# Kernel optimization log

Measured on AMD Instinct MI355X. Metric: run time of the kernel, lower is better.

The kernel has to match this reference:

```python
import jax, jax.numpy as jnp
import numpy as np

NEG_INF = -9e15
ALPHA = 0.2  # LeakyReLU negative slope


def setup_inputs() -> dict:
    key = jax.random.key(0)
    k1, k2, k3, k4 = jax.random.split(key, 4)
    B, N, C_IN, C_OUT, H = 8, 2048, 256, 256, 4
    node_feats = jax.random.normal(k1, (B, N, C_IN), dtype=jnp.float32)
    adj_matrix = jax.random.randint(k2, (B, N, N), 0, 2, dtype=jnp.int32)
    # include self-connections as the docstring expects
    eye = jnp.eye(N, dtype=jnp.int32)[None]
    adj_matrix = jnp.maximum(adj_matrix, eye)
    W = jax.random.normal(k3, (C_OUT, C_IN), dtype=jnp.float32) * (1.414 / np.sqrt(C_IN))
    b = jnp.zeros((C_OUT,), dtype=jnp.float32)
    a = jax.random.normal(k4, (H, 2 * (C_OUT // H)), dtype=jnp.float32) * 0.1
    return {"node_feats": node_feats, "adj_matrix": adj_matrix, "W": W, "b": b, "a": a}


def reference(node_feats, adj_matrix, W, b, a):
    B, N, _ = node_feats.shape
    H, two_c = a.shape
    c = two_c // 2
    # projection: [B, N, H, c]
    f = (jnp.einsum('bni,oi->bno', node_feats, W) + b).reshape(B, N, H, c)
    # attention logit for edge (i, j): leakyrelu(a . [f_i, f_j])
    # decomposes as leakyrelu(s_src[i] + s_dst[j])
    a_src, a_dst = a[:, :c], a[:, c:]
    s_src = jnp.einsum('bnhc,hc->bnh', f, a_src)  # [B, N, H]
    s_dst = jnp.einsum('bnhc,hc->bnh', f, a_dst)  # [B, N, H]
    logits = jax.nn.leaky_relu(s_src[:, :, None, :] + s_dst[:, None, :, :], ALPHA)  # [B,N,N,H]
    logits = jnp.where(adj_matrix[..., None] == 1, logits, NEG_INF)
    probs = jax.nn.softmax(logits, axis=2)  # softmax over source nodes j
    out = jnp.einsum('bijh,bjhc->bihc', probs, f)
    return out.reshape(B, N, H * c)  # concat_heads=True
```

## Files before the change

kernel.cpp:

```cpp
#include <hip/hip_runtime.h>

#define LOG2E 1.4426950408889634f

typedef __attribute__((ext_vector_type(8))) short short8;
typedef __attribute__((ext_vector_type(4))) float f32x4;

__device__ __forceinline__ unsigned short f2bf(float f) {
  unsigned int u = __float_as_uint(f);
  u = (u + 0x7fffu + ((u >> 16) & 1u)) >> 16;
  return (unsigned short)u;
}

__global__ __launch_bounds__(256) void gat_k1(
    const float* __restrict__ X, const float* __restrict__ W,
    const float* __restrict__ bias, const float* __restrict__ a,
    unsigned short* __restrict__ ft, float* __restrict__ ssrc,
    float* __restrict__ sdst)
{
  __shared__ float Xs[8][128];
  __shared__ float Ws[8][128];
  const int tid = threadIdx.x;
  const int tx = tid & 15, ty = tid >> 4;
  const int m0 = blockIdx.x * 128;
  const int c0 = blockIdx.y * 128;

  float acc[8][8];
#pragma unroll
  for (int r = 0; r < 8; ++r)
#pragma unroll
    for (int j = 0; j < 8; ++j) acc[r][j] = 0.f;

  const int lrow = tid >> 1;
  const int kk0 = (tid & 1) * 4;
  const float* Xp = X + (size_t)(m0 + lrow) * 256 + kk0;
  const float* Wp = W + (size_t)(c0 + lrow) * 256 + kk0;

  for (int kc = 0; kc < 256; kc += 8) {
    float4 xv = *(const float4*)(Xp + kc);
    float4 wv = *(const float4*)(Wp + kc);
    __syncthreads();
    Xs[kk0 + 0][lrow] = xv.x; Xs[kk0 + 1][lrow] = xv.y;
    Xs[kk0 + 2][lrow] = xv.z; Xs[kk0 + 3][lrow] = xv.w;
    Ws[kk0 + 0][lrow] = wv.x; Ws[kk0 + 1][lrow] = wv.y;
    Ws[kk0 + 2][lrow] = wv.z; Ws[kk0 + 3][lrow] = wv.w;
    __syncthreads();
#pragma unroll
    for (int kk = 0; kk < 8; ++kk) {
      float av[8], wv8[8];
#pragma unroll
      for (int r = 0; r < 8; ++r) av[r] = Xs[kk][ty * 8 + r];
#pragma unroll
      for (int j = 0; j < 8; ++j) wv8[j] = Ws[kk][tx * 8 + j];
#pragma unroll
      for (int r = 0; r < 8; ++r)
#pragma unroll
        for (int j = 0; j < 8; ++j) acc[r][j] = fmaf(av[r], wv8[j], acc[r][j]);
    }
  }

  const int b = m0 >> 11;
  const int nloc0 = (m0 & 2047) + ty * 8;
  const int cg0 = c0 + tx * 8;
  const int h = cg0 >> 6;
  const int cb = cg0 & 63;

  float bv[8], av_s[8], av_d[8];
#pragma unroll
  for (int j = 0; j < 8; ++j) {
    bv[j]   = bias[cg0 + j];
    av_s[j] = a[h * 128 + cb + j];
    av_d[j] = a[h * 128 + 64 + cb + j];
  }
#pragma unroll
  for (int r = 0; r < 8; ++r)
#pragma unroll
    for (int j = 0; j < 8; ++j) acc[r][j] += bv[j];

  const int jt = nloc0 >> 4;
  const int ni = nloc0 & 15;
#pragma unroll
  for (int j = 0; j < 8; ++j) {
    unsigned int u[4];
#pragma unroll
    for (int q = 0; q < 4; ++q) {
      unsigned int lo = f2bf(acc[2 * q + 0][j]);
      unsigned int hi = f2bf(acc[2 * q + 1][j]);
      u[q] = lo | (hi << 16);
    }
    size_t off = ((((size_t)b * 128 + jt) * 4 + h) * 64 + (cb + j)) * 16 + ni;
    *(uint4*)(ft + off) = make_uint4(u[0], u[1], u[2], u[3]);
  }

  float sp[8], dp[8];
#pragma unroll
  for (int r = 0; r < 8; ++r) {
    float s = 0.f, d = 0.f;
#pragma unroll
    for (int j = 0; j < 8; ++j) {
      s = fmaf(acc[r][j], av_s[j], s);
      d = fmaf(acc[r][j], av_d[j], d);
    }
    sp[r] = s; dp[r] = d;
  }
#pragma unroll
  for (int off = 1; off < 8; off <<= 1) {
#pragma unroll
    for (int r = 0; r < 8; ++r) {
      sp[r] += __shfl_xor(sp[r], off);
      dp[r] += __shfl_xor(dp[r], off);
    }
  }
  if ((tx & 7) == 0) {
    float* sb = ssrc + ((size_t)b * 4 + h) * 2048 + nloc0;
    float* db = sdst + ((size_t)b * 4 + h) * 2048 + nloc0;
#pragma unroll
    for (int r = 0; r < 8; ++r) { sb[r] = sp[r] * LOG2E; db[r] = dp[r] * LOG2E; }
  }
}

__global__ __launch_bounds__(512, 8) void gat_k2(
    const int* __restrict__ adj, const unsigned short* __restrict__ ft,
    const float* __restrict__ ssrc, const float* __restrict__ sdst,
    float* __restrict__ out)
{
  __shared__ __align__(16) unsigned char lds[37120];
  float* sd = (float*)lds;
  unsigned* Aw = (unsigned*)(lds + 32768);

  const int tid = threadIdx.x;
  const int b = blockIdx.x & 7;
  const int itile = blockIdx.x >> 3;
  const int i0 = itile * 16;
  const int w = tid >> 6;
  const int h = w >> 1;
  const int p = w & 1;
  const int lane = tid & 63;
  const int i_l = lane & 15;
  const int kg = lane >> 4;
  const int shamt = kg * 8;

  {
    const float4* src = (const float4*)(sdst + (size_t)b * 4 * 2048);
    float4* dst = (float4*)sd;
#pragma unroll
    for (int q = 0; q < 4; ++q) dst[tid + q * 512] = src[tid + q * 512];
  }
  {
    const int* abase = adj + (size_t)b * 2048 * 2048 + (size_t)i0 * 2048;
    unsigned short* dst16 = (unsigned short*)Aw;
#pragma unroll
    for (int k = 0; k < 4; ++k) {
      const int idx = k * 512 + tid;
      const int r = idx >> 7;
      const int s16 = idx & 127;
      const int4* ap = (const int4*)(abase + (size_t)r * 2048 + s16 * 16);
      int4 v0 = ap[0], v1 = ap[1], v2 = ap[2], v3 = ap[3];
      int vv[16] = {v0.x, v0.y, v0.z, v0.w, v1.x, v1.y, v1.z, v1.w,
                    v2.x, v2.y, v2.z, v2.w, v3.x, v3.y, v3.z, v3.w};
      unsigned m = 0;
#pragma unroll
      for (int i = 0; i < 16; ++i) m |= (vv[i] ? 1u : 0u) << i;
      dst16[((s16 >> 1) * 17 + r) * 2 + (s16 & 1)] = (unsigned short)m;
    }
  }
  const float si = ssrc[((size_t)b * 4 + h) * 2048 + i0 + i_l];
  const float* sdh = sd + h * 2048 + p * 1024 + kg * 8;
  const unsigned short* ftb =
      ft + ((((size_t)b * 128 + p * 64 + (kg >> 1)) * 4 + h) * 64 + i_l) * 16 +
      (kg & 1) * 8;

  f32x4 acc0, acc1, acc2, acc3;
#pragma unroll
  for (int q = 0; q < 4; ++q) { acc0[q] = 0.f; acc1[q] = 0.f; acc2[q] = 0.f; acc3[q] = 0.f; }
  float lsum = 0.f;

  __syncthreads();

#define COMP(s)                                                   \
  {                                                               \
    const unsigned wrd = Aw[(p * 32 + (s)) * 17 + i_l];           \
    const unsigned byte_ = (wrd >> shamt) & 0xffu;                \
    const float* tp_ = sdh + (s) * 32;                            \
    float4 t0_ = *(const float4*)tp_;                             \
    float4 t1_ = *(const float4*)(tp_ + 4);                       \
    float tj_[8] = {t0_.x, t0_.y, t0_.z, t0_.w,                   \
                    t1_.x, t1_.y, t1_.z, t1_.w};                  \
    float e_[8];                                                  \
    _Pragma("unroll")                                             \
    for (int q = 0; q < 8; ++q) {                                 \
      float x_ = si + tj_[q];                                     \
      float y_ = fmaxf(x_, 0.2f * x_);                            \
      float ev_ = __builtin_amdgcn_exp2f(y_);                     \
      ev_ = (byte_ & (1u << q)) ? ev_ : 0.f;                      \
      e_[q] = ev_;                                                \
      lsum += ev_;                                                \
    }                                                             \
    union { unsigned u[4]; short8 v; } af_;                       \
    _Pragma("unroll")                                             \
    for (int q2 = 0; q2 < 4; ++q2) {                              \
      unsigned r_;                                                \
      asm("v_cvt_pk_bf16_f32 %0, %1, %2"                          \
          : "=v"(r_) : "v"(e_[2 * q2]), "v"(e_[2 * q2 + 1]));     \
      af_.u[q2] = r_;                                             \
    }                                                             \
    const unsigned short* fp_ = ftb + (size_t)(s) * 8192;         \
    union { uint4 q; short8 v; } b0_, b1_, b2_, b3_;              \
    b0_.q = *(const uint4*)(fp_);                                 \
    b1_.q = *(const uint4*)(fp_ + 256);                           \
    b2_.q = *(const uint4*)(fp_ + 512);                           \
    b3_.q = *(const uint4*)(fp_ + 768);                           \
    acc0 = __builtin_amdgcn_mfma_f32_16x16x32_bf16(af_.v, b0_.v, acc0, 0, 0, 0); \
    acc1 = __builtin_amdgcn_mfma_f32_16x16x32_bf16(af_.v, b1_.v, acc1, 0, 0, 0); \
    acc2 = __builtin_amdgcn_mfma_f32_16x16x32_bf16(af_.v, b2_.v, acc2, 0, 0, 0); \
    acc3 = __builtin_amdgcn_mfma_f32_16x16x32_bf16(af_.v, b3_.v, acc3, 0, 0, 0); \
  }

#pragma unroll 4
  for (int s = 0; s < 32; ++s) {
    COMP(s)
  }
#undef COMP

  float lsum2 = lsum + __shfl_xor(lsum, 16);
  lsum2 += __shfl_xor(lsum2, 32);
  float* ep = (float*)lds;
  float* el = (float*)(lds + 16384);
  __syncthreads();
  if (p == 1) {
#pragma unroll
    for (int r = 0; r < 4; ++r) {
      const int row = kg * 4 + r;
      ep[(h * 16 + row) * 64 + 0  + i_l] = acc0[r];
      ep[(h * 16 + row) * 64 + 16 + i_l] = acc1[r];
      ep[(h * 16 + row) * 64 + 32 + i_l] = acc2[r];
      ep[(h * 16 + row) * 64 + 48 + i_l] = acc3[r];
    }
    if (lane < 16) el[h * 16 + lane] = lsum2;
  }
  __syncthreads();
  if (p == 0) {
    const float L = lsum2 + el[h * 16 + i_l];
    const float rinv = 1.0f / L;
    float* ob = out + ((size_t)(b * 2048 + i0)) * 256 + h * 64;
#pragma unroll
    for (int r = 0; r < 4; ++r) {
      const int row = kg * 4 + r;
      const float ri = __shfl(rinv, row);
      ob[(size_t)row * 256 + 0  + i_l] = (acc0[r] + ep[(h * 16 + row) * 64 + 0  + i_l]) * ri;
      ob[(size_t)row * 256 + 16 + i_l] = (acc1[r] + ep[(h * 16 + row) * 64 + 16 + i_l]) * ri;
      ob[(size_t)row * 256 + 32 + i_l] = (acc2[r] + ep[(h * 16 + row) * 64 + 32 + i_l]) * ri;
      ob[(size_t)row * 256 + 48 + i_l] = (acc3[r] + ep[(h * 16 + row) * 64 + 48 + i_l]) * ri;
    }
  }
}

extern "C" void kernel_launch(void* const* d_in, const int* in_sizes, int n_in,
                              void* d_out, int out_size, void* d_ws, size_t ws_size,
                              hipStream_t stream) {
  const float* X    = (const float*)d_in[0];
  const int*   adj  = (const int*)d_in[1];
  const float* W    = (const float*)d_in[2];
  const float* bias = (const float*)d_in[3];
  const float* a    = (const float*)d_in[4];
  float* out = (float*)d_out;

  unsigned short* ft = (unsigned short*)d_ws;
  float* ssrc = (float*)((char*)d_ws + 8388608);
  float* sdst = ssrc + 8 * 4 * 2048;

  gat_k1<<<dim3(128, 2, 1), 256, 0, stream>>>(X, W, bias, a, ft, ssrc, sdst);
  gat_k2<<<dim3(1024, 1, 1), 512, 0, stream>>>(adj, ft, ssrc, sdst, out);
}
```

Before: 106.5 us.

## Software-pipeline feature and mask loads in attention aggregation loop

Measured after the change: 106.6 us. About the same (+0.0%).

```diff
diff --git a/kernel.cpp b/kernel.cpp
--- a/kernel.cpp
+++ b/kernel.cpp
@@ -4,6 +4,9 @@
 
 typedef __attribute__((ext_vector_type(8))) short short8;
 typedef __attribute__((ext_vector_type(4))) float f32x4;
+
+union AF { unsigned u[4]; short8 v; };
+union BB { uint4 q; short8 v; };
 
 __device__ __forceinline__ unsigned short f2bf(float f) {
   unsigned int u = __float_as_uint(f);
@@ -118,7 +121,7 @@
   }
 }
 
-__global__ __launch_bounds__(512, 8) void gat_k2(
+__global__ __launch_bounds__(512, 5) void gat_k2(
     const int* __restrict__ adj, const unsigned short* __restrict__ ft,
     const float* __restrict__ ssrc, const float* __restrict__ sdst,
     float* __restrict__ out)
@@ -139,6 +142,22 @@
   const int kg = lane >> 4;
   const int shamt = kg * 8;
 
+  const unsigned short* ftb =
+      ft + ((((size_t)b * 128 + p * 64 + (kg >> 1)) * 4 + h) * 64 + i_l) * 16 +
+      (kg & 1) * 8;
+
+  uint4 A0, A1, A2, A3, B0, B1, B2, B3;
+#define LOADB(s, P0_, P1_, P2_, P3_)                               \
+  {                                                                \
+    const unsigned short* fp_ = ftb + (size_t)(s) * 8192;          \
+    P0_ = *(const uint4*)(fp_);                                    \
+    P1_ = *(const uint4*)(fp_ + 256);                              \
+    P2_ = *(const uint4*)(fp_ + 512);                              \
+    P3_ = *(const uint4*)(fp_ + 768);                              \
+  }
+  LOADB(0, A0, A1, A2, A3)
+  LOADB(1, B0, B1, B2, B3)
+
   {
     const float4* src = (const float4*)(sdst + (size_t)b * 4 * 2048);
     float4* dst = (float4*)sd;
@@ -165,61 +184,91 @@
   }
   const float si = ssrc[((size_t)b * 4 + h) * 2048 + i0 + i_l];
   const float* sdh = sd + h * 2048 + p * 1024 + kg * 8;
-  const unsigned short* ftb =
-      ft + ((((size_t)b * 128 + p * 64 + (kg >> 1)) * 4 + h) * 64 + i_l) * 16 +
-      (kg & 1) * 8;
 
   f32x4 acc0, acc1, acc2, acc3;
 #pragma unroll
   for (int q = 0; q < 4; ++q) { acc0[q] = 0.f; acc1[q] = 0.f; acc2[q] = 0.f; acc3[q] = 0.f; }
-  float lsum = 0.f;
+  float lsumA = 0.f, lsumB = 0.f;
 
   __syncthreads();
 
-#define COMP(s)                                                   \
-  {                                                               \
-    const unsigned wrd = Aw[(p * 32 + (s)) * 17 + i_l];           \
-    const unsigned byte_ = (wrd >> shamt) & 0xffu;                \
-    const float* tp_ = sdh + (s) * 32;                            \
-    float4 t0_ = *(const float4*)tp_;                             \
-    float4 t1_ = *(const float4*)(tp_ + 4);                       \
-    float tj_[8] = {t0_.x, t0_.y, t0_.z, t0_.w,                   \
-                    t1_.x, t1_.y, t1_.z, t1_.w};                  \
-    float e_[8];                                                  \
-    _Pragma("unroll")                                             \
-    for (int q = 0; q < 8; ++q) {                                 \
-      float x_ = si + tj_[q];                                     \
-      float y_ = fmaxf(x_, 0.2f * x_);                            \
-      float ev_ = __builtin_amdgcn_exp2f(y_);                     \
-      ev_ = (byte_ & (1u << q)) ? ev_ : 0.f;                      \
-      e_[q] = ev_;                                                \
-      lsum += ev_;                                                \
-    }                                                             \
-    union { unsigned u[4]; short8 v; } af_;                       \
-    _Pragma("unroll")                                             \
-    for (int q2 = 0; q2 < 4; ++q2) {                              \
-      unsigned r_;                                                \
-      asm("v_cvt_pk_bf16_f32 %0, %1, %2"                          \
-          : "=v"(r_) : "v"(e_[2 * q2]), "v"(e_[2 * q2 + 1]));     \
-      af_.u[q2] = r_;                                             \
-    }                                                             \
-    const unsigned short* fp_ = ftb + (size_t)(s) * 8192;         \
-    union { uint4 q; short8 v; } b0_, b1_, b2_, b3_;              \
-    b0_.q = *(const uint4*)(fp_);                                 \
-    b1_.q = *(const uint4*)(fp_ + 256);                           \
-    b2_.q = *(const uint4*)(fp_ + 512);                           \
-    b3_.q = *(const uint4*)(fp_ + 768);                           \
-    acc0 = __builtin_amdgcn_mfma_f32_16x16x32_bf16(af_.v, b0_.v, acc0, 0, 0, 0); \
-    acc1 = __builtin_amdgcn_mfma_f32_16x16x32_bf16(af_.v, b1_.v, acc1, 0, 0, 0); \
-    acc2 = __builtin_amdgcn_mfma_f32_16x16x32_bf16(af_.v, b2_.v, acc2, 0, 0, 0); \
-    acc3 = __builtin_amdgcn_mfma_f32_16x16x32_bf16(af_.v, b3_.v, acc3, 0, 0, 0); \
-  }
-
-#pragma unroll 4
-  for (int s = 0; s < 32; ++s) {
-    COMP(s)
-  }
-#undef COMP
+#define LOADM(s, mw_, t0_, t1_)                                    \
+  {                                                                \
+    mw_ = Aw[(p * 32 + (s)) * 17 + i_l];                           \
+    const float* tp_ = sdh + (size_t)(s) * 32;                     \
+    t0_ = *(const float4*)tp_;                                     \
+    t1_ = *(const float4*)(tp_ + 4);                               \
+  }
+
+#define COMPE(mw_, t0_, t1_, af_, lsum_)                           \
+  {                                                                \
+    const unsigned byte_ = ((mw_) >> shamt) & 0xffu;               \
+    float tj_[8] = {t0_.x, t0_.y, t0_.z, t0_.w,                    \
+                    t1_.x, t1_.y, t1_.z, t1_.w};                   \
+    float e_[8];                                                   \
+    _Pragma("unroll")                                              \
+    for (int q = 0; q < 8; ++q) {                                  \
+      float x_ = si + tj_[q];                                      \
+      float y_ = fmaxf(x_, 0.2f * x_);                             \
+      float ev_ = __builtin_amdgcn_exp2f(y_);                      \
+      e_[q] = (byte_ & (1u << q)) ? ev_ : 0.f;                     \
+    }                                                              \
+    float s01_ = e_[0] + e_[1], s23_ = e_[2] + e_[3];              \
+    float s45_ = e_[4] + e_[5], s67_ = e_[6] + e_[7];              \
+    lsum_ += (s01_ + s23_) + (s45_ + s67_);                        \
+    _Pragma("unroll")                                              \
+    for (int q2 = 0; q2 < 4; ++q2) {                               \
+      unsigned r_;                                                 \
+      asm("v_cvt_pk_bf16_f32 %0, %1, %2"                           \
+          : "=v"(r_) : "v"(e_[2 * q2]), "v"(e_[2 * q2 + 1]));      \
+      af_.u[q2] = r_;                                              \
+    }                                                              \
+  }
+
+#define DOMFMA(af_, P0_, P1_, P2_, P3_)                            \
+  {                                                                \
+    BB bb_;                                                        \
+    bb_.q = P0_;                                                   \
+    acc0 = __builtin_amdgcn_mfma_f32_16x16x32_bf16(af_.v, bb_.v, acc0, 0, 0, 0); \
+    bb_.q = P1_;                                                   \
+    acc1 = __builtin_amdgcn_mfma_f32_16x16x32_bf16(af_.v, bb_.v, acc1, 0, 0, 0); \
+    bb_.q = P2_;                                                   \
+    acc2 = __builtin_amdgcn_mfma_f32_16x16x32_bf16(af_.v, bb_.v, acc2, 0, 0, 0); \
+    bb_.q = P3_;                                                   \
+    acc3 = __builtin_amdgcn_mfma_f32_16x16x32_bf16(af_.v, bb_.v, acc3, 0, 0, 0); \
+  }
+
+  unsigned mwA, mwB;
+  float4 ta0, ta1, tb0, tb1;
+  LOADM(0, mwA, ta0, ta1)
+
+  for (int s = 0; s < 32; s += 2) {
+    LOADM(s + 1, mwB, tb0, tb1)
+    AF afA;
+    COMPE(mwA, ta0, ta1, afA, lsumA)
+    DOMFMA(afA, A0, A1, A2, A3)
+    {
+      const int sn = (s + 2 < 32) ? s + 2 : 31;
+      LOADB(sn, A0, A1, A2, A3)
+    }
+    {
+      const int sm = (s + 2 < 32) ? s + 2 : 31;
+      LOADM(sm, mwA, ta0, ta1)
+    }
+    AF afB;
+    COMPE(mwB, tb0, tb1, afB, lsumB)
+    DOMFMA(afB, B0, B1, B2, B3)
+    {
+      const int sn = (s + 3 < 32) ? s + 3 : 31;
+      LOADB(sn, B0, B1, B2, B3)
+    }
+  }
+#undef LOADB
+#undef LOADM
+#undef COMPE
+#undef DOMFMA
+
+  float lsum = lsumA + lsumB;
 
   float lsum2 = lsum + __shfl_xor(lsum, 16);
   lsum2 += __shfl_xor(lsum2, 32);
```
